# Kernel optimization log

Hardware: AMD Instinct MI355X
Metric: run time of the kernel (lower is better)

## Reference

```python
import jax, jax.numpy as jnp
import numpy as np

N = 100000   # nodes
E = 1600000  # edges
G = 64       # graphs in batch
F_IN = 128
HID = 128
CLS = 10
K = 3


def _cheb_norm(edge_index, n):
    # PyG ChebConv norm with sym normalization, lambda_max=2.0:
    # L_hat = 2L/lambda_max - I = -D^-1/2 A D^-1/2 (diagonal cancels to 0)
    src, dst = edge_index[0], edge_index[1]
    ones = jnp.ones((edge_index.shape[1],), jnp.float32)
    deg = jax.ops.segment_sum(ones, src, num_segments=n)
    dinv = jnp.where(deg > 0, jax.lax.rsqrt(jnp.maximum(deg, 1.0)), 0.0)
    w = -dinv[src] * dinv[dst]  # [E]
    return src, dst, w


def _prop(x, src, dst, w, n):
    # out[i] = sum_{e: dst[e]=i} w[e] * x[src[e]]
    return jax.ops.segment_sum(w[:, None] * x[src], dst, num_segments=n)


def _cheb_conv(x, W, b, src, dst, w, n):
    # W: [K, in, out]; Chebyshev recurrence T0=x, T1=Lhat x, Tk=2 Lhat T_{k-1} - T_{k-2}
    Tx0 = x
    out = Tx0 @ W[0]
    Tx1 = _prop(Tx0, src, dst, w, n)
    out = out + Tx1 @ W[1]
    for k in range(2, W.shape[0]):
        Tx2 = 2.0 * _prop(Tx1, src, dst, w, n) - Tx0
        out = out + Tx2 @ W[k]
        Tx0, Tx1 = Tx1, Tx2
    return out + b


def setup_inputs() -> dict:
    key = jax.random.key(0)
    ks = jax.random.split(key, 12)
    x = jax.random.normal(ks[0], (N, F_IN), jnp.float32)
    edge_index = jax.random.randint(ks[1], (2, E), 0, N, jnp.int32)
    batch = jnp.sort(jax.random.randint(ks[2], (N,), 0, G, jnp.int32))
    s1 = (1.0 / np.sqrt(F_IN)).astype(np.float32) if False else 1.0 / np.sqrt(F_IN)
    s2 = 1.0 / np.sqrt(HID)
    W1 = jax.random.uniform(ks[3], (K, F_IN, HID), jnp.float32, -s1, s1)
    b1 = jnp.zeros((HID,), jnp.float32)
    W2 = jax.random.uniform(ks[4], (K, HID, HID), jnp.float32, -s2, s2)
    b2 = jnp.zeros((HID,), jnp.float32)
    W3 = jax.random.uniform(ks[5], (K, HID, HID), jnp.float32, -s2, s2)
    b3 = jnp.zeros((HID,), jnp.float32)
    Wl = jax.random.uniform(ks[6], (HID, CLS), jnp.float32, -s2, s2)
    bl = jnp.zeros((CLS,), jnp.float32)
    return {"x": x, "edge_index": edge_index, "batch": batch,
            "W1": W1, "b1": b1, "W2": W2, "b2": b2, "W3": W3, "b3": b3,
            "Wl": Wl, "bl": bl}


def reference(x, edge_index, batch, W1, b1, W2, b2, W3, b3, Wl, bl):
    src, dst, w = _cheb_norm(edge_index, N)
    h = jax.nn.relu(_cheb_conv(x, W1, b1, src, dst, w, N))
    h = jax.nn.relu(_cheb_conv(h, W2, b2, src, dst, w, N))
    h = _cheb_conv(h, W3, b3, src, dst, w, N)
    # global_mean_pool over variable-size graphs
    sums = jax.ops.segment_sum(h, batch, num_segments=G)
    cnts = jax.ops.segment_sum(jnp.ones((N,), jnp.float32), batch, num_segments=G)
    pooled = sums / jnp.maximum(cnts, 1.0)[:, None]
    # dropout p=0.5 is identity in eval mode
    return pooled @ Wl + bl
```

## Files before the change

### kernel.cpp

```cpp
#include <hip/hip_runtime.h>
#include <cstdint>
#include <cstddef>

#define FDIM 128
#define CLSN 10
#define RCAP 64

#define BSH 7
#define BN  (1 << BSH)
#define NBUCK 782
#define BCAP 4096
#define DEGC 128

typedef __attribute__((ext_vector_type(2))) float f32x2;
typedef __attribute__((ext_vector_type(4))) float f32x4;
typedef __attribute__((ext_vector_type(4))) _Float16 h16x4;
typedef __attribute__((ext_vector_type(8))) _Float16 h16x8;

#if defined(__has_builtin)
#if __has_builtin(__builtin_amdgcn_cvt_pk_f32_fp8) && __has_builtin(__builtin_amdgcn_cvt_pk_fp8_f32)
#define NATIVE_FP8 1
#endif
#endif

union hbits { unsigned short u; _Float16 h; };

#ifdef NATIVE_FP8
#define FP8_POSTSCALE 1.0f
__device__ __forceinline__ void dec8(uint2 p, float* f) {
  auto r0 = __builtin_amdgcn_cvt_pk_f32_fp8((int)p.x, false);
  auto r1 = __builtin_amdgcn_cvt_pk_f32_fp8((int)p.x, true);
  auto r2 = __builtin_amdgcn_cvt_pk_f32_fp8((int)p.y, false);
  auto r3 = __builtin_amdgcn_cvt_pk_f32_fp8((int)p.y, true);
  f[0] = r0[0]; f[1] = r0[1]; f[2] = r1[0]; f[3] = r1[1];
  f[4] = r2[0]; f[5] = r2[1]; f[6] = r3[0]; f[7] = r3[1];
}
__device__ __forceinline__ unsigned enc4(const float* f) {
  int a = __builtin_amdgcn_cvt_pk_fp8_f32(f[0], f[1], 0, false);
  a = __builtin_amdgcn_cvt_pk_fp8_f32(f[2], f[3], a, true);
  return (unsigned)a;
}
__device__ __forceinline__ uint2 enc8(const float* f) {
  return make_uint2(enc4(f), enc4(f + 4));
}
#else
#define FP8_POSTSCALE 256.0f
__device__ __forceinline__ float dec1(unsigned b) {
  hbits t;
  t.u = (unsigned short)(((b & 0x80u) << 8) | ((b & 0x7Fu) << 7));
  return (float)t.h;
}
__device__ __forceinline__ void dec8(uint2 p, float* f) {
#pragma unroll
  for (int i = 0; i < 4; ++i) {
    f[i]     = dec1((p.x >> (8 * i)) & 0xFFu);
    f[i + 4] = dec1((p.y >> (8 * i)) & 0xFFu);
  }
}
__device__ __forceinline__ unsigned enc1(float v) {
  hbits t;
  t.h = (_Float16)(v * 0.00390625f);
  unsigned short b = t.u;
  unsigned mag = b & 0x7FFFu;
  unsigned r = (mag + 0x3Fu + ((mag >> 7) & 1u)) >> 7;
  if (r > 0x7Eu) r = 0x7Eu;
  return ((b >> 8) & 0x80u) | r;
}
__device__ __forceinline__ unsigned enc4(const float* f) {
  unsigned lo = 0;
#pragma unroll
  for (int i = 0; i < 4; ++i) lo |= enc1(f[i]) << (8 * i);
  return lo;
}
__device__ __forceinline__ uint2 enc8(const float* f) {
  return make_uint2(enc4(f), enc4(f + 4));
}
#endif

__device__ __forceinline__ void dec16(uint4 p, float* f) {
  dec8(make_uint2(p.x, p.y), f);
  dec8(make_uint2(p.z, p.w), f + 8);
}

__device__ __forceinline__ void acc16(uint4 p, f32x2* a) {
#ifdef NATIVE_FP8
  {
    auto r = __builtin_amdgcn_cvt_pk_f32_fp8((int)p.x, false);
    a[0][0] += r[0]; a[0][1] += r[1];
  }
  {
    auto r = __builtin_amdgcn_cvt_pk_f32_fp8((int)p.x, true);
    a[1][0] += r[0]; a[1][1] += r[1];
  }
  {
    auto r = __builtin_amdgcn_cvt_pk_f32_fp8((int)p.y, false);
    a[2][0] += r[0]; a[2][1] += r[1];
  }
  {
    auto r = __builtin_amdgcn_cvt_pk_f32_fp8((int)p.y, true);
    a[3][0] += r[0]; a[3][1] += r[1];
  }
  {
    auto r = __builtin_amdgcn_cvt_pk_f32_fp8((int)p.z, false);
    a[4][0] += r[0]; a[4][1] += r[1];
  }
  {
    auto r = __builtin_amdgcn_cvt_pk_f32_fp8((int)p.z, true);
    a[5][0] += r[0]; a[5][1] += r[1];
  }
  {
    auto r = __builtin_amdgcn_cvt_pk_f32_fp8((int)p.w, false);
    a[6][0] += r[0]; a[6][1] += r[1];
  }
  {
    auto r = __builtin_amdgcn_cvt_pk_f32_fp8((int)p.w, true);
    a[7][0] += r[0]; a[7][1] += r[1];
  }
#else
  float f[16];
  dec16(p, f);
#pragma unroll
  for (int j = 0; j < 8; ++j) { a[j][0] += f[2 * j]; a[j][1] += f[2 * j + 1]; }
#endif
}

__global__ __launch_bounds__(256) void deg_hist_kernel(
    const int* __restrict__ src, unsigned* __restrict__ degp,
    int nw, int nwh, int E) {
  __shared__ unsigned hist[12544];
  const int k = blockIdx.x >> 1, h = blockIdx.x & 1;
  const int wbase = h * nwh;
  for (int i = threadIdx.x; i < nwh; i += 256) hist[i] = 0;
  __syncthreads();
  int chunk = (E + DEGC - 1) / DEGC;
  int e0 = k * chunk, e1 = min(e0 + chunk, E);
  for (int e = e0 + threadIdx.x; e < e1; e += 256) {
    int s = src[e];
    int wl = (s >> 2) - wbase;
    if ((unsigned)wl < (unsigned)nwh)
      atomicAdd(&hist[wl], 1u << (8 * (s & 3)));
  }
  __syncthreads();
  unsigned* out = degp + (size_t)k * nw + wbase;
  int lim = min(nwh, nw - wbase);
  for (int i = threadIdx.x; i < lim; i += 256) out[i] = hist[i];
}

__global__ void dinv_kernel(const unsigned* __restrict__ degp,
                            float* __restrict__ dinv, float* __restrict__ rsc,
                            int nw) {
  int w = blockIdx.x * blockDim.x + threadIdx.x;
  if (w >= nw) return;
  unsigned acc = 0;
#pragma unroll 4
  for (int k = 0; k < DEGC; ++k) acc += degp[(size_t)k * nw + w];
  float4 o, r;
  {
    int d0 = (int)(acc & 0xFFu);
    int d1 = (int)((acc >> 8) & 0xFFu);
    int d2 = (int)((acc >> 16) & 0xFFu);
    int d3 = (int)((acc >> 24) & 0xFFu);
    o.x = d0 > 0 ? rsqrtf((float)d0) : 0.f;
    o.y = d1 > 0 ? rsqrtf((float)d1) : 0.f;
    o.z = d2 > 0 ? rsqrtf((float)d2) : 0.f;
    o.w = d3 > 0 ? rsqrtf((float)d3) : 0.f;
    r.x = FP8_POSTSCALE * sqrtf((float)d0);
    r.y = FP8_POSTSCALE * sqrtf((float)d1);
    r.z = FP8_POSTSCALE * sqrtf((float)d2);
    r.w = FP8_POSTSCALE * sqrtf((float)d3);
  }
  *(float4*)(dinv + (size_t)w * 4) = o;
  *(float4*)(rsc + (size_t)w * 4) = r;
}

__global__ __launch_bounds__(256) void partA_kernel(
    const int* __restrict__ src, const int* __restrict__ dst,
    int* __restrict__ bfill, unsigned* __restrict__ bedges, int E) {
  __shared__ int cnt[NBUCK];
  __shared__ int run[NBUCK];
  int chunk = (E + gridDim.x - 1) / gridDim.x;
  int e0 = blockIdx.x * chunk;
  int e1 = min(e0 + chunk, E);
  for (int i = threadIdx.x; i < NBUCK; i += 256) cnt[i] = 0;
  __syncthreads();
  for (int e = e0 + threadIdx.x; e < e1; e += 256)
    atomicAdd(&cnt[dst[e] >> BSH], 1);
  __syncthreads();
  for (int i = threadIdx.x; i < NBUCK; i += 256) {
    int c = cnt[i];
    run[i] = c ? atomicAdd(&bfill[i], c) : 0;
  }
  __syncthreads();
  for (int e = e0 + threadIdx.x; e < e1; e += 256) {
    int d = dst[e];
    int b = d >> BSH;
    int off = atomicAdd(&run[b], 1);
    if (off < BCAP)
      bedges[(size_t)b * BCAP + off] =
          ((unsigned)(d & (BN - 1)) << 17) | (unsigned)src[e];
  }
}

__global__ __launch_bounds__(256) void partB_kernel(
    const unsigned* __restrict__ bedges, const int* __restrict__ bfill,
    int* __restrict__ rows, int* __restrict__ fillc, int n) {
  __shared__ int img[BN * RCAP];
  __shared__ unsigned ncnt[BN];
  int b = blockIdx.x;
  for (int i = threadIdx.x; i < BN; i += 256) ncnt[i] = 0;
  for (int i = threadIdx.x; i < BN * RCAP; i += 256) img[i] = n;
  __syncthreads();
  int m = bfill[b]; if (m > BCAP) m = BCAP;
  const unsigned* be = bedges + (size_t)b * BCAP;
  for (int i = threadIdx.x; i < m; i += 256) {
    unsigned p = be[i];
    int dl = (int)(p >> 17);
    int s = (int)(p & 0x1FFFFu);
    unsigned slot = atomicAdd(&ncnt[dl], 1u);
    if (slot < RCAP) img[dl * RCAP + slot] = s;
  }
  __syncthreads();
  int node0 = b << BSH;
  for (int i = threadIdx.x; i < BN * RCAP; i += 256) {
    int node = node0 + (i >> 6);
    if (node < n) rows[(size_t)node * RCAP + (i & 63)] = img[i];
  }
  if (threadIdx.x < BN) {
    int node = node0 + threadIdx.x;
    if (node < n) fillc[node] = (int)ncnt[threadIdx.x];
  }
}

__global__ __launch_bounds__(256) void aux_kernel(
    const float* __restrict__ x, _Float16* __restrict__ xh, unsigned char* __restrict__ x8,
    unsigned char* __restrict__ y8, const float* __restrict__ dinv,
    const float* __restrict__ W1, const float* __restrict__ W2, const float* __restrict__ W3,
    _Float16* __restrict__ Gh, int n) {
  const int MS = FDIM * FDIM;
  int id = blockIdx.x * blockDim.x + threadIdx.x;
  int nc = n * (FDIM / 8);
  if (id < nc) {
    float4 v0 = *(const float4*)(x + (size_t)id * 8);
    float4 v1 = *(const float4*)(x + (size_t)id * 8 + 4);
    float f[8] = {v0.x, v0.y, v0.z, v0.w, v1.x, v1.y, v1.z, v1.w};
    h16x8 h = {(_Float16)f[0], (_Float16)f[1], (_Float16)f[2], (_Float16)f[3],
               (_Float16)f[4], (_Float16)f[5], (_Float16)f[6], (_Float16)f[7]};
    *(h16x8*)(xh + (size_t)id * 8) = h;
    float dv = dinv[id >> 4];
    float g[8];
#pragma unroll
    for (int j = 0; j < 8; ++j) g[j] = dv * f[j];
    *(uint2*)(x8 + (size_t)id * 8) = enc8(g);
    return;
  }
  id -= nc;
  if (id < 3 * 3 * MS) {
    int L = id / (3 * MS);
    int rem = id - L * 3 * MS;
    int S = rem / MS;
    int e = rem - S * MS;
    int k = e >> 7, nn = e & 127;
    const float* W = (L == 0) ? W1 : (L == 1) ? W2 : W3;
    float w0 = W[e], w1 = W[MS + e], w2 = W[2 * MS + e];
    float v = (S == 0) ? (w0 - w2) : (S == 1) ? w1 : (2.f * w2);
    int c = k >> 5, q = (k >> 3) & 3, j = k & 7;
    int w = nn >> 6, nl = (nn >> 2) & 15, r = nn & 3;
    int t = w * 4 + r;
    int lane = q * 16 + nl;
    size_t o = ((((size_t)(L * 3 + S) * 4 + c) * 8 + t) * 64 + lane) * 8 + j;
    Gh[o] = (_Float16)v;
    return;
  }
  id -= 3 * 3 * MS;
  if (id < 32) {
    unsigned char* dstp = (id < 16) ? x8 : y8;
    ((uint2*)(dstp + (size_t)n * FDIM))[id & 15] = make_uint2(0u, 0u);
  }
}

__global__ __launch_bounds__(256) void prop_kernel(
    const unsigned char* __restrict__ x8, unsigned char* __restrict__ out8,
    const float* __restrict__ dinv,
    const int* __restrict__ rcnt, const int* __restrict__ rows, int n) {
  const int lane = threadIdx.x & 63;
  const int g = lane >> 3, fl = lane & 7;
  int wid = (int)(((size_t)blockIdx.x * blockDim.x + threadIdx.x) >> 6);
  int node = wid * 8 + g;
  if (node >= n) return;
  int m = rcnt[node]; if (m > RCAP) m = RCAP;
  const int* __restrict__ row = rows + (size_t)node * RCAP;
  const unsigned char* __restrict__ xf = x8 + fl * 16;
  f32x2 acc[8];
#pragma unroll
  for (int j = 0; j < 8; ++j) acc[j] = (f32x2){0.f, 0.f};

  int2 rr = *(const int2*)row;
  for (int e = 0; e < m; e += 2) {
    int2 pp = *(const int2*)(row + e + 2);
    uint4 v0 = *(const uint4*)(xf + (size_t)rr.x * FDIM);
    uint4 v1 = *(const uint4*)(xf + (size_t)rr.y * FDIM);
    acc16(v0, acc);
    acc16(v1, acc);
    rr = pp;
  }

  float dv = dinv[node];
  float q = -dv * dv * FP8_POSTSCALE;
  float u[16];
#pragma unroll
  for (int j = 0; j < 8; ++j) {
    u[2 * j]     = q * acc[j][0];
    u[2 * j + 1] = q * acc[j][1];
  }
  uint2 a = enc8(u), b = enc8(u + 8);
  *(uint4*)(out8 + (size_t)node * FDIM + fl * 16) = make_uint4(a.x, a.y, b.x, b.y);
}

#define GBM 128
#define APAD 40
__global__ __launch_bounds__(256) void gemm3_mfma_kernel(
    const _Float16* __restrict__ A0, const unsigned char* __restrict__ A1_8,
    const unsigned char* __restrict__ A2_8,
    const _Float16* __restrict__ Gh,
    const float* __restrict__ bias, const float* __restrict__ rsc,
    _Float16* __restrict__ C16, unsigned char* __restrict__ C8,
    const float* __restrict__ dinv,
    int n, int layer, int do_relu) {
  __shared__ _Float16 a_s[GBM * APAD];
  const int tid = threadIdx.x;
  const int lane = tid & 63;
  const int wave = tid >> 6;
  const int wm = wave >> 1, wn = wave & 1;
  const int bm0 = blockIdx.x * GBM;
  const int lm = lane & 15, lq = lane >> 4;

  f32x4 acc[4][4];
#pragma unroll
  for (int mt = 0; mt < 4; ++mt)
#pragma unroll
    for (int nt = 0; nt < 4; ++nt) acc[mt][nt] = (f32x4){0.f, 0.f, 0.f, 0.f};

#pragma unroll 1
  for (int c = 0; c < 4; ++c) {
    __syncthreads();
#pragma unroll
    for (int i = 0; i < 2; ++i) {
      int id = tid + i * 256;
      int row = id >> 2, cg = (id & 3) * 8;
      int gr = bm0 + row; if (gr >= n) gr = n - 1;
      h16x8 v = *(const h16x8*)(A0 + (size_t)gr * FDIM + c * 32 + cg);
      *(h16x8*)&a_s[row * APAD + cg] = v;
    }
    __syncthreads();
    h16x8 af[4];
#pragma unroll
    for (int mt = 0; mt < 4; ++mt) {
      int r = wm * 64 + mt * 16 + lm;
      af[mt] = *(const h16x8*)&a_s[r * APAD + lq * 8];
    }
    h16x8 bh[4];
    size_t gb = (((size_t)(layer * 3 + 0) * 4 + c) * 8) * 512;
#pragma unroll
    for (int nt = 0; nt < 4; ++nt) {
      int t = wn * 4 + nt;
      bh[nt] = *(const h16x8*)(Gh + gb + ((size_t)t * 64 + lane) * 8);
    }
#pragma unroll
    for (int mt = 0; mt < 4; ++mt)
#pragma unroll
      for (int nt = 0; nt < 4; ++nt)
        acc[mt][nt] = __builtin_amdgcn_mfma_f32_16x16x32_f16(af[mt], bh[nt], acc[mt][nt], 0, 0, 0);
  }

#pragma unroll 1
  for (int S = 1; S < 3; ++S) {
    const unsigned char* __restrict__ A8 = (S == 1) ? A1_8 : A2_8;
#pragma unroll 1
    for (int c = 0; c < 4; ++c) {
      __syncthreads();
#pragma unroll
      for (int i = 0; i < 2; ++i) {
        int id = tid + i * 256;
        int row = id >> 2, cg = (id & 3) * 8;
        int gr = bm0 + row; if (gr >= n) gr = n - 1;
        uint2 p = *(const uint2*)(A8 + (size_t)gr * FDIM + c * 32 + cg);
        float f[8];
        dec8(p, f);
        float s = rsc[gr];
        h16x8 v = {(_Float16)(f[0] * s), (_Float16)(f[1] * s),
                   (_Float16)(f[2] * s), (_Float16)(f[3] * s),
                   (_Float16)(f[4] * s), (_Float16)(f[5] * s),
                   (_Float16)(f[6] * s), (_Float16)(f[7] * s)};
        *(h16x8*)&a_s[row * APAD + cg] = v;
      }
      __syncthreads();
      h16x8 af[4];
#pragma unroll
      for (int mt = 0; mt < 4; ++mt) {
        int r = wm * 64 + mt * 16 + lm;
        af[mt] = *(const h16x8*)&a_s[r * APAD + lq * 8];
      }
      h16x8 bh[4];
      size_t gb = (((size_t)(layer * 3 + S) * 4 + c) * 8) * 512;
#pragma unroll
      for (int nt = 0; nt < 4; ++nt) {
        int t = wn * 4 + nt;
        bh[nt] = *(const h16x8*)(Gh + gb + ((size_t)t * 64 + lane) * 8);
      }
#pragma unroll
      for (int mt = 0; mt < 4; ++mt)
#pragma unroll
        for (int nt = 0; nt < 4; ++nt)
          acc[mt][nt] = __builtin_amdgcn_mfma_f32_16x16x32_f16(af[mt], bh[nt], acc[mt][nt], 0, 0, 0);
    }
  }

  const int col0 = wn * 64 + lm * 4;
  float4 bvec = *(const float4*)(bias + col0);
  float bv[4] = {bvec.x, bvec.y, bvec.z, bvec.w};
#pragma unroll
  for (int mt = 0; mt < 4; ++mt) {
#pragma unroll
    for (int r = 0; r < 4; ++r) {
      int row = bm0 + wm * 64 + mt * 16 + lq * 4 + r;
      if (row < n) {
        float v[4];
#pragma unroll
        for (int nt = 0; nt < 4; ++nt) {
          float t = acc[mt][nt][r] + bv[nt];
          v[nt] = do_relu ? fmaxf(t, 0.f) : t;
        }
        h16x4 hv = {(_Float16)v[0], (_Float16)v[1], (_Float16)v[2], (_Float16)v[3]};
        *(h16x4*)(C16 + (size_t)row * FDIM + col0) = hv;
        if (C8) {
          float dv = dinv[row];
          float vs[4] = {dv * v[0], dv * v[1], dv * v[2], dv * v[3]};
          *(unsigned*)(C8 + (size_t)row * FDIM + col0) = enc4(vs);
        }
      }
    }
  }
}

__device__ __forceinline__ int lb_search(const int* __restrict__ b, int n, int val) {
  int lo = 0, hi = n;
  while (lo < hi) { int mid = (lo + hi) >> 1; if (b[mid] < val) lo = mid + 1; else hi = mid; }
  return lo;
}

#define PSPL 16
__global__ __launch_bounds__(256) void pool_kernel(
    const _Float16* __restrict__ h, const int* __restrict__ batch,
    float* __restrict__ sums, int* __restrict__ cntg, int n) {
  int g = blockIdx.x, s = blockIdx.y;
  int beg = lb_search(batch, n, g);
  int end = lb_search(batch, n, g + 1);
  if (s == 0 && threadIdx.x == 0) cntg[g] = end - beg;
  long long len = end - beg;
  int c0 = beg + (int)((len * s) / PSPL);
  int c1 = beg + (int)((len * (s + 1)) / PSPL);
  int chunk = threadIdx.x & 15;
  int rq = threadIdx.x >> 4;
  float acc[8];
#pragma unroll
  for (int j = 0; j < 8; ++j) acc[j] = 0.f;
  for (int r = c0 + rq; r < c1; r += 16) {
    h16x8 v = *(const h16x8*)(h + (size_t)r * FDIM + chunk * 8);
#pragma unroll
    for (int j = 0; j < 8; ++j) acc[j] += (float)v[j];
  }
#pragma unroll
  for (int j = 0; j < 8; ++j) {
    acc[j] += __shfl_xor(acc[j], 16);
    acc[j] += __shfl_xor(acc[j], 32);
  }
  __shared__ float sh[4][16][8];
  int wave = threadIdx.x >> 6, lane = threadIdx.x & 63;
  if (lane < 16) {
#pragma unroll
    for (int j = 0; j < 8; ++j) sh[wave][lane][j] = acc[j];
  }
  __syncthreads();
  if (threadIdx.x < 128) {
    int ch = threadIdx.x >> 3, j = threadIdx.x & 7;
    float v = sh[0][ch][j] + sh[1][ch][j] + sh[2][ch][j] + sh[3][ch][j];
    if (v != 0.f || c1 > c0) atomicAdd(&sums[g * FDIM + ch * 8 + j], v);
  }
}

__global__ void final_kernel(const float* __restrict__ sums, const int* __restrict__ cntg,
                             const float* __restrict__ Wl, const float* __restrict__ bl,
                             float* __restrict__ out) {
  int g = blockIdx.x;
  __shared__ float row[FDIM];
  int t = threadIdx.x;
  float inv = 1.f / fmaxf((float)cntg[g], 1.f);
  row[t] = sums[g * FDIM + t] * inv;
  __syncthreads();
  if (t < CLSN) {
    float a = bl[t];
#pragma unroll 4
    for (int f = 0; f < FDIM; ++f) a = fmaf(row[f], Wl[f * CLSN + t], a);
    out[g * CLSN + t] = a;
  }
}

extern "C" void kernel_launch(void* const* d_in, const int* in_sizes, int n_in,
                              void* d_out, int out_size, void* d_ws, size_t ws_size,
                              hipStream_t stream) {
  const float* x   = (const float*)d_in[0];
  const int*   ei  = (const int*)d_in[1];
  const int* batch = (const int*)d_in[2];
  const float* W1  = (const float*)d_in[3];
  const float* b1  = (const float*)d_in[4];
  const float* W2  = (const float*)d_in[5];
  const float* b2  = (const float*)d_in[6];
  const float* W3  = (const float*)d_in[7];
  const float* b3  = (const float*)d_in[8];
  const float* Wl  = (const float*)d_in[9];
  const float* bl  = (const float*)d_in[10];
  float* out = (float*)d_out;

  const int n = in_sizes[0] / FDIM;
  const int E = in_sizes[1] / 2;
  const int nw = (n + 3) / 4;
  const int nwh = (nw + 1) / 2;
  const int* esrc = ei;
  const int* edst = ei + E;

  char* ws = (char*)d_ws;
  size_t off = 0;
  auto alloc = [&](size_t bytes) -> void* {
    void* p = ws + off;
    off += (bytes + 255) & ~(size_t)255;
    return p;
  };
  const size_t NH = (size_t)n * FDIM * sizeof(_Float16);
  const size_t N8 = (size_t)(n + 1) * FDIM;
  _Float16* Ha16 = (_Float16*)alloc(NH);
  unsigned char* Ha8 = (unsigned char*)alloc(N8);
  unsigned char* Hb8 = (unsigned char*)alloc(N8);
  unsigned char* Hc8 = (unsigned char*)alloc(N8);
  int*      rows = (int*)alloc((size_t)n * RCAP * 4 + 32);
  int*      fillc = (int*)alloc((size_t)n * 4);
  float*    dinv = (float*)alloc((size_t)nw * 16);
  float*    rsc  = (float*)alloc((size_t)nw * 16);
  _Float16* Gh   = (_Float16*)alloc((size_t)3 * 3 * FDIM * FDIM * 2);
  unsigned* degp = (unsigned*)alloc((size_t)DEGC * nw * 4);
  unsigned* bedges = (unsigned*)alloc((size_t)NBUCK * BCAP * 4);
  char*  zbase = ws + off;
  int*   bfill = (int*)alloc((size_t)NBUCK * 4);
  float* sums  = (float*)alloc((size_t)64 * FDIM * 4);
  int*   cntg  = (int*)alloc((size_t)64 * 4);
  size_t zsize = (size_t)((ws + off) - zbase);
  hipMemsetAsync(zbase, 0, zsize, stream);

  deg_hist_kernel<<<DEGC * 2, 256, 0, stream>>>(esrc, degp, nw, nwh, E);
  partA_kernel<<<256, 256, 0, stream>>>(esrc, edst, bfill, bedges, E);
  dinv_kernel<<<(nw + 255) / 256, 256, 0, stream>>>(degp, dinv, rsc, nw);
  partB_kernel<<<NBUCK, 256, 0, stream>>>(bedges, bfill, rows, fillc, n);
  int aux_items = n * (FDIM / 8) + 3 * 3 * FDIM * FDIM + 32;
  aux_kernel<<<(aux_items + 255) / 256, 256, 0, stream>>>(x, Ha16, Ha8, Hb8, dinv,
                                                          W1, W2, W3, Gh, n);

  int prop_grid = (n + 31) / 32;
  int gemm_grid = (n + GBM - 1) / GBM;

  prop_kernel<<<prop_grid, 256, 0, stream>>>(Ha8, Hb8, dinv, fillc, rows, n);
  prop_kernel<<<prop_grid, 256, 0, stream>>>(Hb8, Hc8, dinv, fillc, rows, n);
  gemm3_mfma_kernel<<<gemm_grid, 256, 0, stream>>>(Ha16, Hb8, Hc8, Gh, b1, rsc,
                                                   Ha16, Ha8, dinv, n, 0, 1);

  prop_kernel<<<prop_grid, 256, 0, stream>>>(Ha8, Hb8, dinv, fillc, rows, n);
  prop_kernel<<<prop_grid, 256, 0, stream>>>(Hb8, Hc8, dinv, fillc, rows, n);
  gemm3_mfma_kernel<<<gemm_grid, 256, 0, stream>>>(Ha16, Hb8, Hc8, Gh, b2, rsc,
                                                   Ha16, Ha8, dinv, n, 1, 1);

  prop_kernel<<<prop_grid, 256, 0, stream>>>(Ha8, Hb8, dinv, fillc, rows, n);
  prop_kernel<<<prop_grid, 256, 0, stream>>>(Hb8, Hc8, dinv, fillc, rows, n);
  gemm3_mfma_kernel<<<gemm_grid, 256, 0, stream>>>(Ha16, Hb8, Hc8, Gh, b3, rsc,
                                                   Ha16, nullptr, dinv, n, 2, 0);

  pool_kernel<<<dim3(64, PSPL), 256, 0, stream>>>(Ha16, batch, sums, cntg, n);
  final_kernel<<<64, 128, 0, stream>>>(sums, cntg, Wl, bl, out);
}
```

Measured before the change: 525.8 us.

## Drop LDS staging in gemm3; each wave owns 32 rows across all columns

The fused three-term GEMM kernel no longer stages the A tile through shared memory with barriers. Each wave now takes 32 rows by all 128 output columns and loads its A fragments straight from global memory into registers, with the per-row scale hoisted out of the loop. The chunk loops are fully unrolled so loads can overlap MFMAs. This removes LDS traffic and __syncthreads but reuses each B fragment across only two row tiles instead of four, raising B loads per MFMA, and the A loads become narrower, less coalesced global reads.

Measured after the change: 594.1 us. 13.0% more time.

```diff
diff --git a/kernel.cpp b/kernel.cpp
--- a/kernel.cpp
+++ b/kernel.cpp
@@ -317,7 +317,6 @@
 }
 
 #define GBM 128
-#define APAD 40
 __global__ __launch_bounds__(256) void gemm3_mfma_kernel(
     const _Float16* __restrict__ A0, const unsigned char* __restrict__ A1_8,
     const unsigned char* __restrict__ A2_8,
@@ -326,116 +325,100 @@
     _Float16* __restrict__ C16, unsigned char* __restrict__ C8,
     const float* __restrict__ dinv,
     int n, int layer, int do_relu) {
-  __shared__ _Float16 a_s[GBM * APAD];
   const int tid = threadIdx.x;
   const int lane = tid & 63;
-  const int wave = tid >> 6;
-  const int wm = wave >> 1, wn = wave & 1;
+  const int wm = tid >> 6;
   const int bm0 = blockIdx.x * GBM;
   const int lm = lane & 15, lq = lane >> 4;
 
-  f32x4 acc[4][4];
-#pragma unroll
-  for (int mt = 0; mt < 4; ++mt)
-#pragma unroll
-    for (int nt = 0; nt < 4; ++nt) acc[mt][nt] = (f32x4){0.f, 0.f, 0.f, 0.f};
-
-#pragma unroll 1
+  f32x4 acc[2][8];
+#pragma unroll
+  for (int mt = 0; mt < 2; ++mt)
+#pragma unroll
+    for (int nt = 0; nt < 8; ++nt) acc[mt][nt] = (f32x4){0.f, 0.f, 0.f, 0.f};
+
+  int gr[2];
+#pragma unroll
+  for (int mt = 0; mt < 2; ++mt) {
+    int r = bm0 + wm * 32 + mt * 16 + lm;
+    gr[mt] = r < n ? r : n - 1;
+  }
+  float rs[2];
+#pragma unroll
+  for (int mt = 0; mt < 2; ++mt) rs[mt] = rsc[gr[mt]];
+
+#pragma unroll
   for (int c = 0; c < 4; ++c) {
-    __syncthreads();
-#pragma unroll
-    for (int i = 0; i < 2; ++i) {
-      int id = tid + i * 256;
-      int row = id >> 2, cg = (id & 3) * 8;
-      int gr = bm0 + row; if (gr >= n) gr = n - 1;
-      h16x8 v = *(const h16x8*)(A0 + (size_t)gr * FDIM + c * 32 + cg);
-      *(h16x8*)&a_s[row * APAD + cg] = v;
+    h16x8 af[2];
+#pragma unroll
+    for (int mt = 0; mt < 2; ++mt)
+      af[mt] = *(const h16x8*)(A0 + (size_t)gr[mt] * FDIM + c * 32 + lq * 8);
+    const _Float16* gB = Gh + (((size_t)(layer * 3 + 0) * 4 + c) * 8) * 512 + (size_t)lane * 8;
+#pragma unroll
+    for (int t = 0; t < 8; ++t) {
+      h16x8 bh = *(const h16x8*)(gB + (size_t)t * 512);
+#pragma unroll
+      for (int mt = 0; mt < 2; ++mt)
+        acc[mt][t] = __builtin_amdgcn_mfma_f32_16x16x32_f16(af[mt], bh, acc[mt][t], 0, 0, 0);
     }
-    __syncthreads();
-    h16x8 af[4];
-#pragma unroll
-    for (int mt = 0; mt < 4; ++mt) {
-      int r = wm * 64 + mt * 16 + lm;
-      af[mt] = *(const h16x8*)&a_s[r * APAD + lq * 8];
-    }
-    h16x8 bh[4];
-    size_t gb = (((size_t)(layer * 3 + 0) * 4 + c) * 8) * 512;
-#pragma unroll
-    for (int nt = 0; nt < 4; ++nt) {
-      int t = wn * 4 + nt;
-      bh[nt] = *(const h16x8*)(Gh + gb + ((size_t)t * 64 + lane) * 8);
-    }
-#pragma unroll
-    for (int mt = 0; mt < 4; ++mt)
-#pragma unroll
-      for (int nt = 0; nt < 4; ++nt)
-        acc[mt][nt] = __builtin_amdgcn_mfma_f32_16x16x32_f16(af[mt], bh[nt], acc[mt][nt], 0, 0, 0);
   }
 
 #pragma unroll 1
   for (int S = 1; S < 3; ++S) {
     const unsigned char* __restrict__ A8 = (S == 1) ? A1_8 : A2_8;
-#pragma unroll 1
+#pragma unroll
     for (int c = 0; c < 4; ++c) {
-      __syncthreads();
-#pragma unroll
-      for (int i = 0; i < 2; ++i) {
-        int id = tid + i * 256;
-        int row = id >> 2, cg = (id & 3) * 8;
-        int gr = bm0 + row; if (gr >= n) gr = n - 1;
-        uint2 p = *(const uint2*)(A8 + (size_t)gr * FDIM + c * 32 + cg);
+      h16x8 af[2];
+#pragma unroll
+      for (int mt = 0; mt < 2; ++mt) {
+        uint2 p = *(const uint2*)(A8 + (size_t)gr[mt] * FDIM + c * 32 + lq * 8);
         float f[8];
         dec8(p, f);
-        float s = rsc[gr];
-        h16x8 v = {(_Float16)(f[0] * s), (_Float16)(f[1] * s),
-                   (_Float16)(f[2] * s), (_Float16)(f[3] * s),
-                   (_Float16)(f[4] * s), (_Float16)(f[5] * s),
-                   (_Float16)(f[6] * s), (_Float16)(f[7] * s)};
-        *(h16x8*)&a_s[row * APAD + cg] = v;
+        float s = rs[mt];
+        af[mt] = (h16x8){(_Float16)(f[0] * s), (_Float16)(f[1] * s),
+                         (_Float16)(f[2] * s), (_Float16)(f[3] * s),
+                         (_Float16)(f[4] * s), (_Float16)(f[5] * s),
+                         (_Float16)(f[6] * s), (_Float16)(f[7] * s)};
       }
-      __syncthreads();
-      h16x8 af[4];
-#pragma unroll
-      for (int mt = 0; mt < 4; ++mt) {
-        int r = wm * 64 + mt * 16 + lm;
-        af[mt] = *(const h16x8*)&a_s[r * APAD + lq * 8];
+      const _Float16* gB = Gh + (((size_t)(layer * 3 + S) * 4 + c) * 8) * 512 + (size_t)lane * 8;
+#pragma unroll
+      for (int t = 0; t < 8; ++t) {
+        h16x8 bh = *(const h16x8*)(gB + (size_t)t * 512);
+#pragma unroll
+        for (int mt = 0; mt < 2; ++mt)
+          acc[mt][t] = __builtin_amdgcn_mfma_f32_16x16x32_f16(af[mt], bh, acc[mt][t], 0, 0, 0);
       }
-      h16x8 bh[4];
-      size_t gb = (((size_t)(layer * 3 + S) * 4 + c) * 8) * 512;
-#pragma unroll
-      for (int nt = 0; nt < 4; ++nt) {
-        int t = wn * 4 + nt;
-        bh[nt] = *(const h16x8*)(Gh + gb + ((size_t)t * 64 + lane) * 8);
-      }
-#pragma unroll
-      for (int mt = 0; mt < 4; ++mt)
-#pragma unroll
-        for (int nt = 0; nt < 4; ++nt)
-          acc[mt][nt] = __builtin_amdgcn_mfma_f32_16x16x32_f16(af[mt], bh[nt], acc[mt][nt], 0, 0, 0);
     }
   }
 
-  const int col0 = wn * 64 + lm * 4;
-  float4 bvec = *(const float4*)(bias + col0);
-  float bv[4] = {bvec.x, bvec.y, bvec.z, bvec.w};
-#pragma unroll
-  for (int mt = 0; mt < 4; ++mt) {
+  float bv[2][4];
+#pragma unroll
+  for (int w = 0; w < 2; ++w) {
+    float4 b4 = *(const float4*)(bias + w * 64 + lm * 4);
+    bv[w][0] = b4.x; bv[w][1] = b4.y; bv[w][2] = b4.z; bv[w][3] = b4.w;
+  }
+#pragma unroll
+  for (int mt = 0; mt < 2; ++mt) {
 #pragma unroll
     for (int r = 0; r < 4; ++r) {
-      int row = bm0 + wm * 64 + mt * 16 + lq * 4 + r;
+      int row = bm0 + wm * 32 + mt * 16 + lq * 4 + r;
       if (row < n) {
-        float v[4];
-#pragma unroll
-        for (int nt = 0; nt < 4; ++nt) {
-          float t = acc[mt][nt][r] + bv[nt];
-          v[nt] = do_relu ? fmaxf(t, 0.f) : t;
-        }
-        h16x4 hv = {(_Float16)v[0], (_Float16)v[1], (_Float16)v[2], (_Float16)v[3]};
-        *(h16x4*)(C16 + (size_t)row * FDIM + col0) = hv;
-        if (C8) {
-          float dv = dinv[row];
-          float vs[4] = {dv * v[0], dv * v[1], dv * v[2], dv * v[3]};
-          *(unsigned*)(C8 + (size_t)row * FDIM + col0) = enc4(vs);
+        float dvr = C8 ? dinv[row] : 0.f;
+#pragma unroll
+        for (int w = 0; w < 2; ++w) {
+          int col0 = w * 64 + lm * 4;
+          float v[4];
+#pragma unroll
+          for (int j = 0; j < 4; ++j) {
+            float t = acc[mt][w * 4 + j][r] + bv[w][j];
+            v[j] = do_relu ? fmaxf(t, 0.f) : t;
+          }
+          h16x4 hv = {(_Float16)v[0], (_Float16)v[1], (_Float16)v[2], (_Float16)v[3]};
+          *(h16x4*)(C16 + (size_t)row * FDIM + col0) = hv;
+          if (C8) {
+            float vs[4] = {dvr * v[0], dvr * v[1], dvr * v[2], dvr * v[3]};
+            *(unsigned*)(C8 + (size_t)row * FDIM + col0) = enc4(vs);
+          }
         }
       }
     }
```
